# Kernel optimization log

Hardware: AMD Instinct MI355X
Metric: run time of the kernel (lower is better)

## Reference

```python
import jax, jax.numpy as jnp
import numpy as np

BLOCK = 128
FP8_MAX = 448.0


def _quant_weight(w):
    # Per 128x128 block quantization to fp8 e4m3, matching weight.scale layout [N/128, K/128].
    N, K = w.shape
    nb, kb = N // BLOCK, K // BLOCK
    wb = w.reshape(nb, BLOCK, kb, BLOCK)
    s = jnp.max(jnp.abs(wb), axis=(1, 3)) / FP8_MAX  # [nb, kb]
    q = (wb / s[:, None, :, None]).astype(jnp.float8_e4m3fn).astype(jnp.float32)
    return q.reshape(N, K), s


def setup_inputs() -> dict:
    key = jax.random.key(0)
    kx, kw = jax.random.split(key)
    M, K, N = 4096, 4096, 4096
    x = jax.random.normal(kx, (M, K), dtype=jnp.float32)
    w = jax.random.normal(kw, (N, K), dtype=jnp.float32) * 0.02
    w_q, w_s = _quant_weight(w)
    return {"x": x, "w_q": w_q, "w_s": w_s}


def _act_quant(x):
    # Per-row, per-128-element block quantization (act_quant kernel): s = max|x|/448, y = fp8(x/s).
    M, K = x.shape
    kb = K // BLOCK
    xb = x.reshape(M, kb, BLOCK)
    s = jnp.max(jnp.abs(xb), axis=-1) / FP8_MAX  # [M, kb]
    q = (xb / s[..., None]).astype(jnp.float8_e4m3fn).astype(jnp.float32)
    return q.reshape(M, K), s


def reference(x, w_q, w_s):
    # fp8 GEMM with inline block-wise dequant (fp32 accumulation): since the scales are
    # constant within each K-block, accumulating (A_blk @ B_blk^T) * a_s * b_s over blocks
    # equals dequantizing both operands elementwise then one fp32 matmul.
    M, K = x.shape
    N = w_q.shape[0]
    nb, kb = N // BLOCK, K // BLOCK
    x_q, x_s = _act_quant(x)
    a = x_q.reshape(M, kb, BLOCK) * x_s[..., None]                       # dequant activations
    a = a.reshape(M, K)
    b = (w_q.reshape(nb, BLOCK, kb, BLOCK) * w_s[:, None, :, None]).reshape(N, K)  # dequant weights
    return a @ b.T  # [M, N]
```

## Files before the change

kernel.cpp:

```cpp
#include <hip/hip_runtime.h>

typedef float f32x4 __attribute__((ext_vector_type(4)));
typedef int   i32x4 __attribute__((ext_vector_type(4)));
typedef int   i32x8 __attribute__((ext_vector_type(8)));

#define FP8_MAX 448.0f
#define AS1 __attribute__((address_space(1)))
#define AS3 __attribute__((address_space(3)))

__global__ __launch_bounds__(256) void act_quant_k(const float* __restrict__ x,
                                                   unsigned char* __restrict__ xq,
                                                   float* __restrict__ xst,
                                                   int M, int K) {
    const int t   = threadIdx.x;
    const int qb  = blockIdx.x * 8 + (t >> 5);
    const int l32 = t & 31;
    const int row = qb >> 5;
    const int kb  = qb & 31;
    const size_t base = (size_t)row * K + (size_t)kb * 128 + (size_t)l32 * 4;

    float4 v = *(const float4*)(x + base);
    float am = fmaxf(fmaxf(fabsf(v.x), fabsf(v.y)), fmaxf(fabsf(v.z), fabsf(v.w)));
#pragma unroll
    for (int off = 1; off < 32; off <<= 1)
        am = fmaxf(am, __shfl_xor(am, off, 64));

    const float s = am / FP8_MAX;
    const float q0 = v.x / s, q1 = v.y / s, q2 = v.z / s, q3 = v.w / s;
    int p = __builtin_amdgcn_cvt_pk_fp8_f32(q0, q1, 0, false);
    p     = __builtin_amdgcn_cvt_pk_fp8_f32(q2, q3, p, true);
    *(int*)(xq + base) = p;
    if (l32 == 0) xst[(size_t)kb * M + row] = s;
}

__global__ __launch_bounds__(256) void wq_cvt_k(const float* __restrict__ w,
                                                unsigned char* __restrict__ wq) {
    const size_t i = ((size_t)blockIdx.x * 256 + threadIdx.x) * 4;
    float4 v = *(const float4*)(w + i);
    int p = __builtin_amdgcn_cvt_pk_fp8_f32(v.x, v.y, 0, false);
    p     = __builtin_amdgcn_cvt_pk_fp8_f32(v.z, v.w, p, true);
    *(int*)(wq + i) = p;
}

__global__ __launch_bounds__(512, 2) void gemm_fp8_blk(
    const unsigned char* __restrict__ Aq,
    const unsigned char* __restrict__ Bq,
    const float* __restrict__ xst,
    const float* __restrict__ wsc,
    float* __restrict__ C, int M, int N, int K) {
    __shared__ unsigned char As[2][32768];
    __shared__ unsigned char Bs[2][32768];
    __shared__ float Ss[2][256];

    const int t    = threadIdx.x;
    const int lane = t & 63;
    const int wave = t >> 6;
    const int wr   = wave >> 2;
    const int wc   = wave & 3;
    const int bm   = blockIdx.y * 256;
    const int bn   = blockIdx.x * 256;

    const int srow   = t >> 3;
    const int scolsw = (((t & 7) ^ ((t >> 3) & 7)) << 4);
    const unsigned char* gA = Aq + (size_t)(bm + srow) * K + scolsw;
    const unsigned char* gB = Bq + (size_t)(bn + srow) * K + scolsw;
    const float* gS = xst + bm + ((wave & 3) << 6) + lane;
    const int ldsoff = wave << 10;
    const int sSoff  = (wave & 3) << 8;

    const int r15 = lane & 15;
    const int g   = lane >> 4;
    const int km  = r15 & 7;
    const int pc0 = (((2 * g) ^ km) << 4);
    const int pc1 = pc0 ^ 16;
    const int aBase = (wr * 128 + r15) << 7;
    const int bBase = (wc * 64 + r15) << 7;
    const int ssB   = wr * 128 + (g << 2);

    const float* wscp = wsc + (((bn + wc * 64) >> 7) << 5);

#define STG_A(BUF, KB, I)                                                       \
    __builtin_amdgcn_global_load_lds(                                           \
        (const AS1 void*)(gA + (size_t)(I) * 64 * K + ((size_t)(KB) << 7)),     \
        (AS3 void*)(&As[BUF][0] + (I) * 8192 + ldsoff), 16, 0, 0)
#define STG_B(BUF, KB, I)                                                       \
    __builtin_amdgcn_global_load_lds(                                           \
        (const AS1 void*)(gB + (size_t)(I) * 64 * K + ((size_t)(KB) << 7)),     \
        (AS3 void*)(&Bs[BUF][0] + (I) * 8192 + ldsoff), 16, 0, 0)
#define STG_S(KB)                                                               \
    __builtin_amdgcn_global_load_lds(                                           \
        (const AS1 void*)(gS + (size_t)(KB) * M),                               \
        (AS3 void*)((unsigned char*)&Ss[(KB) & 1][0] + sSoff), 4, 0, 0)
#define VMCNT0() asm volatile("s_waitcnt vmcnt(0)" ::: "memory")

#define RD8(PTR, RB) ({                                                         \
    i32x4 lo_ = *(const i32x4*)((PTR) + (RB) + pc0);                            \
    i32x4 hi_ = *(const i32x4*)((PTR) + (RB) + pc1);                            \
    __builtin_shufflevector(lo_, hi_, 0, 1, 2, 3, 4, 5, 6, 7); })

    f32x4 accM[8][4] = {};
    const f32x4 z4 = {0.f, 0.f, 0.f, 0.f};

    STG_S(0);
#pragma unroll
    for (int i = 0; i < 4; ++i) { STG_A(0, 0, i); STG_B(0, 0, i); }
    VMCNT0();
    __builtin_amdgcn_s_barrier();
    asm volatile("" ::: "memory");

#pragma unroll 1
    for (int kb = 0; kb < 32; ++kb) {
        const int buf = kb & 1;
        if (kb < 31) {
            STG_S(kb + 1);
#pragma unroll
            for (int i = 0; i < 4; ++i) { STG_A(buf ^ 1, kb + 1, i); STG_B(buf ^ 1, kb + 1, i); }
        }
        const float wsv = wscp[kb];
        const unsigned char* ap = &As[buf][0];
        const unsigned char* bp = &Bs[buf][0];
        const float* sp = &Ss[buf][0];

        i32x8 pb[4];
#pragma unroll
        for (int n = 0; n < 4; ++n) pb[n] = RD8(bp, bBase + (n << 11));

#pragma unroll
        for (int h = 0; h < 2; ++h) {
            i32x8 pa[4];
            f32x4 sc[4];
#pragma unroll
            for (int mm = 0; mm < 4; ++mm) {
                pa[mm] = RD8(ap, aBase + ((h * 4 + mm) << 11));
                sc[mm] = (*(const f32x4*)(sp + ssB + ((h * 4 + mm) << 4))) * wsv;
            }
            __builtin_amdgcn_s_setprio(1);
#pragma unroll
            for (int mm = 0; mm < 4; ++mm)
#pragma unroll
                for (int n = 0; n < 4; ++n) {
                    f32x4 q = __builtin_amdgcn_mfma_scale_f32_16x16x128_f8f6f4(
                        pa[mm], pb[n], z4, 0, 0,
                        0, 0x7F7F7F7F,
                        0, 0x7F7F7F7F);
                    accM[h * 4 + mm][n] += q * sc[mm];
                }
            __builtin_amdgcn_s_setprio(0);
        }
        VMCNT0();
        __builtin_amdgcn_s_barrier();
        asm volatile("" ::: "memory");
    }

    const int cm = bm + wr * 128 + (g << 2);
    const int cn = bn + wc * 64 + r15;
#pragma unroll
    for (int m = 0; m < 8; ++m)
#pragma unroll
        for (int n = 0; n < 4; ++n) {
            float* cp = C + (size_t)(cm + m * 16) * N + (cn + n * 16);
#pragma unroll
            for (int r = 0; r < 4; ++r) cp[(size_t)r * N] = accM[m][n][r];
        }
#undef STG_A
#undef STG_B
#undef STG_S
#undef VMCNT0
#undef RD8
}

extern "C" void kernel_launch(void* const* d_in, const int* in_sizes, int n_in,
                              void* d_out, int out_size, void* d_ws, size_t ws_size,
                              hipStream_t stream) {
    const float* x   = (const float*)d_in[0];
    const float* wqf = (const float*)d_in[1];
    const float* wsc = (const float*)d_in[2];
    float* out = (float*)d_out;

    const int M = 4096, N = 4096, K = 4096;

    unsigned char* xq  = (unsigned char*)d_ws;
    unsigned char* wq8 = (unsigned char*)d_ws + (size_t)M * K;
    float* xst = (float*)((unsigned char*)d_ws + (size_t)M * K + (size_t)N * K);

    act_quant_k<<<M * (K / 128) / 8, 256, 0, stream>>>(x, xq, xst, M, K);
    wq_cvt_k<<<(N / 4) * (K / 256), 256, 0, stream>>>(wqf, wq8);
    dim3 grid(N / 256, M / 256);
    gemm_fp8_blk<<<grid, 512, 0, stream>>>(xq, wq8, xst, wsc, out, M, N, K);
}
```

Measured before the change: 126.5 us.

## Software-pipeline LDS fragment reads against MFMAs in quarter steps

Restructures the inner K-block loop so A fragments and scales are read from LDS in quarters, with two slots double-buffered in registers. Each quarter's reads are issued before the previous quarter's MFMAs, hiding LDS latency behind matrix work. The global-to-LDS prefetch is moved after the first LDS reads are issued. The MFMA results for a pair are produced first and scaled afterwards, which adds temporary registers and may raise register pressure under launch_bounds(512,2).

```diff
diff --git a/kernel.cpp b/kernel.cpp
--- a/kernel.cpp
+++ b/kernel.cpp
@@ -98,6 +98,34 @@
     i32x4 hi_ = *(const i32x4*)((PTR) + (RB) + pc1);                            \
     __builtin_shufflevector(lo_, hi_, 0, 1, 2, 3, 4, 5, 6, 7); })
 
+#define ISSUE_Q(SLOT, QQ) do {                                                  \
+    pa[SLOT][0]  = RD8(ap, aBase + ((2 * (QQ)) << 11));                         \
+    pa[SLOT][1]  = RD8(ap, aBase + ((2 * (QQ) + 1) << 11));                     \
+    scr[SLOT][0] = *(const f32x4*)(sp + ssB + ((2 * (QQ)) << 4));               \
+    scr[SLOT][1] = *(const f32x4*)(sp + ssB + ((2 * (QQ) + 1) << 4));           \
+} while (0)
+
+#define MFMA_Q(SLOT, QQ) do {                                                   \
+    f32x4 q_[2][4];                                                             \
+    __builtin_amdgcn_s_setprio(1);                                              \
+    _Pragma("unroll")                                                           \
+    for (int n = 0; n < 4; ++n) {                                               \
+        q_[0][n] = __builtin_amdgcn_mfma_scale_f32_16x16x128_f8f6f4(            \
+            pa[SLOT][0], pb[n], z4, 0, 0, 0, 0x7F7F7F7F, 0, 0x7F7F7F7F);        \
+        q_[1][n] = __builtin_amdgcn_mfma_scale_f32_16x16x128_f8f6f4(            \
+            pa[SLOT][1], pb[n], z4, 0, 0, 0, 0x7F7F7F7F, 0, 0x7F7F7F7F);        \
+    }                                                                           \
+    __builtin_amdgcn_s_setprio(0);                                              \
+    {                                                                           \
+        f32x4 s0_ = scr[SLOT][0] * wsv, s1_ = scr[SLOT][1] * wsv;               \
+        _Pragma("unroll")                                                       \
+        for (int n = 0; n < 4; ++n) {                                           \
+            accM[2 * (QQ)][n]     += q_[0][n] * s0_;                            \
+            accM[2 * (QQ) + 1][n] += q_[1][n] * s1_;                            \
+        }                                                                       \
+    }                                                                           \
+} while (0)
+
     f32x4 accM[8][4] = {};
     const f32x4 z4 = {0.f, 0.f, 0.f, 0.f};
 
@@ -111,42 +139,31 @@
 #pragma unroll 1
     for (int kb = 0; kb < 32; ++kb) {
         const int buf = kb & 1;
-        if (kb < 31) {
-            STG_S(kb + 1);
-#pragma unroll
-            for (int i = 0; i < 4; ++i) { STG_A(buf ^ 1, kb + 1, i); STG_B(buf ^ 1, kb + 1, i); }
-        }
         const float wsv = wscp[kb];
         const unsigned char* ap = &As[buf][0];
         const unsigned char* bp = &Bs[buf][0];
         const float* sp = &Ss[buf][0];
 
         i32x8 pb[4];
+        i32x8 pa[2][2];
+        f32x4 scr[2][2];
+
 #pragma unroll
         for (int n = 0; n < 4; ++n) pb[n] = RD8(bp, bBase + (n << 11));
-
-#pragma unroll
-        for (int h = 0; h < 2; ++h) {
-            i32x8 pa[4];
-            f32x4 sc[4];
-#pragma unroll
-            for (int mm = 0; mm < 4; ++mm) {
-                pa[mm] = RD8(ap, aBase + ((h * 4 + mm) << 11));
-                sc[mm] = (*(const f32x4*)(sp + ssB + ((h * 4 + mm) << 4))) * wsv;
-            }
-            __builtin_amdgcn_s_setprio(1);
-#pragma unroll
-            for (int mm = 0; mm < 4; ++mm)
-#pragma unroll
-                for (int n = 0; n < 4; ++n) {
-                    f32x4 q = __builtin_amdgcn_mfma_scale_f32_16x16x128_f8f6f4(
-                        pa[mm], pb[n], z4, 0, 0,
-                        0, 0x7F7F7F7F,
-                        0, 0x7F7F7F7F);
-                    accM[h * 4 + mm][n] += q * sc[mm];
-                }
-            __builtin_amdgcn_s_setprio(0);
+        ISSUE_Q(0, 0);
+        ISSUE_Q(1, 1);
+        if (kb < 31) {
+            STG_S(kb + 1);
+#pragma unroll
+            for (int i = 0; i < 4; ++i) { STG_A(buf ^ 1, kb + 1, i); STG_B(buf ^ 1, kb + 1, i); }
         }
+        MFMA_Q(0, 0);
+        ISSUE_Q(0, 2);
+        MFMA_Q(1, 1);
+        ISSUE_Q(1, 3);
+        MFMA_Q(0, 2);
+        MFMA_Q(1, 3);
+
         VMCNT0();
         __builtin_amdgcn_s_barrier();
         asm volatile("" ::: "memory");
@@ -167,6 +184,8 @@
 #undef STG_S
 #undef VMCNT0
 #undef RD8
+#undef ISSUE_Q
+#undef MFMA_Q
 }
 
 extern "C" void kernel_launch(void* const* d_in, const int* in_sizes, int n_in,
```

After: 140.4 us. +11.0%, slower.
